# Performance work log

Measured on AMD Instinct MI355X. Metric: run time of the kernel, lower is better.

The kernel has to match this reference:

```python
import jax, jax.numpy as jnp
import numpy as np

# Sizes
N, T, P, D = 1000, 4, 10, 13          # nodes, point types, edge types (T*(T+1)/2), basis dim per point
F, H, EA, K, E = 128, 128, 16, 64, 20000  # node feat, edge hidden, edge attr/feat, edge op bottleneck, edges
I_NODE = D * (D + 1) // 2             # 91: symmetric ('ij=ji') self-block irreps dim
I_EDGE = D * D                        # 169: generic ('ij') block irreps dim
AVG_NEIGH = 20.0


def setup_inputs() -> dict:
    ks = jax.random.split(jax.random.key(0), 16)
    Fin = H + 2 * F                   # edge-op input: [edge_msg, node_h_i, node_h_j]
    return {
        'node_feats': jax.random.normal(ks[0], (N, F), jnp.float32),
        'node_attrs': jax.random.uniform(ks[1], (N, T), dtype=jnp.float32),
        'edge_feats': jax.random.normal(ks[2], (E, EA), jnp.float32),
        'edge_attrs': jax.random.normal(ks[3], (E, EA), jnp.float32),
        'edge_index': jax.random.randint(ks[4], (2, E), 0, N),
        'node_types': jax.random.randint(ks[5], (N,), 0, T),
        'edge_types': jax.random.randint(ks[6], (E,), 0, P),
        'W_msg': jax.random.normal(ks[7], (F, F), jnp.float32) / np.float32(np.sqrt(F)),
        'W_attr': jax.random.normal(ks[8], (T, F), jnp.float32) / np.float32(np.sqrt(T)),
        'W_em': jax.random.normal(ks[9], (2 * F + 2 * EA, H), jnp.float32) / np.float32(np.sqrt(2 * F + 2 * EA)),
        'W_proj': jax.random.normal(ks[10], (Fin, K), jnp.float32) / np.float32(np.sqrt(Fin)),
        'W_node': jax.random.normal(ks[11], (T, F, I_NODE), jnp.float32) / np.float32(np.sqrt(F)),
        'W_edge': jax.random.normal(ks[12], (P, K, I_EDGE), jnp.float32) / np.float32(np.sqrt(K)),
        'cob_node': jax.random.normal(ks[13], (T, I_NODE, D, D), jnp.float32) / np.float32(D),
        'cob_edge': jax.random.normal(ks[14], (P, I_EDGE, D, D), jnp.float32) / np.float32(D),
    }


def reference(node_feats, node_attrs, edge_feats, edge_attrs, edge_index, node_types,
              edge_types, W_msg, W_attr, W_em, W_proj, W_node, W_edge, cob_node, cob_edge):
    src, dst = edge_index[0], edge_index[1]
    # --- node message passing (NodeMessageBlock, simplified linear-aggregate form) ---
    m = node_feats @ W_msg                                             # [N, F]
    agg = jax.ops.segment_sum(m[src], dst, num_segments=N) \
        + jax.ops.segment_sum(m[dst], src, num_segments=N)             # symmetric edge list: both dirs
    node_h = node_feats + agg / AVG_NEIGH + node_attrs @ W_attr        # [N, F]
    # --- edge messages (EdgeMessageBlock, simplified) ---
    e_in = jnp.concatenate([node_h[src], node_h[dst], edge_feats, edge_attrs], axis=-1)
    edge_msg = jnp.tanh(e_in @ W_em)                                   # [E, H]
    # --- self-interaction blocks: per-type gather -> op -> einsum('ni,ixy->nxy', ., cob) ---
    node_irred = jnp.einsum('nf,nfi->ni', node_h, W_node[node_types])  # [N, I_NODE]
    node_blocks = jnp.einsum('ni,nixy->nxy', node_irred, cob_node[node_types])  # [N, D, D]
    # --- interaction blocks: per-edge-type op + change of basis, transpose-symmetrized ---
    onehot = jax.nn.one_hot(edge_types, P, dtype=node_feats.dtype)     # [E, P] type selector

    def edge_block(a, b):
        h = jnp.concatenate([edge_msg, a, b], axis=-1) @ W_proj        # [E, K]
        irr = jnp.einsum('epi,ep->ei', jnp.einsum('ek,pki->epi', h, W_edge), onehot)  # [E, I_EDGE]
        return jnp.einsum('epxy,ep->exy', jnp.einsum('ei,pixy->epxy', irr, cob_edge), onehot)  # [E, D, D]

    blk_ij = edge_block(node_h[src], node_h[dst])
    blk_ji = edge_block(node_h[dst], node_h[src])
    edge_blocks = 0.5 * (blk_ij + jnp.swapaxes(blk_ji, -1, -2))        # symm_transpose
    # --- scatter blocks into the dense symmetric block matrix ---
    off = jnp.arange(D)
    nidx = jnp.arange(N)[:, None] * D + off                            # [N, D] diagonal block rows/cols
    rs = src[:, None] * D + off                                        # [E, D]
    cs = dst[:, None] * D + off
    M = jnp.zeros((N * D, N * D), node_feats.dtype)
    M = M.at[nidx[:, :, None], nidx[:, None, :]].add(node_blocks)
    M = M.at[rs[:, :, None], cs[:, None, :]].add(edge_blocks)
    M = M.at[cs[:, :, None], rs[:, None, :]].add(jnp.swapaxes(edge_blocks, -1, -2))
    return M
```

## Files before the change

kernel.cpp:

```cpp
#include <hip/hip_runtime.h>
#include <cmath>

#define NN   1000
#define TT   4
#define PP   10
#define DD   13
#define FF   128
#define HH   128
#define EAA  16
#define KDIM 64
#define EE   20000
#define I_NODE 91
#define I_EDGE 169
#define MROW  13000
#define OUT_FLOAT4 42250000L

#define WS_M     0L
#define WS_AGG   128000L
#define WS_V1    256000L
#define WS_V2    384000L
#define WS_U     512000L
#define WS_HMSG  640000L
#define WS_WCOMB 1920000L
#define WS_WNC   2028160L

#define NB_CE   640
#define NB_CN   512
#define NB_MSG  1000
#define NB_FRONT (NB_CE + NB_CN + NB_MSG)

__global__ __launch_bounds__(256) void k_front(
    const float* __restrict__ We, const float* __restrict__ cobE,
    const float* __restrict__ Wn, const float* __restrict__ cobN,
    const float* __restrict__ nf, const float* __restrict__ Wmsg,
    float* __restrict__ Wcomb, float* __restrict__ Wnc,
    float* __restrict__ m, float* __restrict__ agg) {
  int b = blockIdx.x, t = threadIdx.x;
  if (b < NB_CE) {
    if (t < I_EDGE) {
      int pk = b, p = pk >> 6;
      float acc = 0.f;
      const float* wrow = We + pk * I_EDGE;
      const float* crow = cobE + p * I_EDGE * I_EDGE + t;
      for (int i = 0; i < I_EDGE; ++i) acc += wrow[i] * crow[i * I_EDGE];
      Wcomb[pk * I_EDGE + t] = acc;
    }
  } else if (b < NB_CE + NB_CN) {
    if (t < I_EDGE) {
      int tf = b - NB_CE, ty = tf >> 7;
      float acc = 0.f;
      const float* wrow = Wn + tf * I_NODE;
      const float* crow = cobN + ty * I_NODE * I_EDGE + t;
      for (int i = 0; i < I_NODE; ++i) acc += wrow[i] * crow[i * I_EDGE];
      Wnc[tf * I_EDGE + t] = acc;
    }
  } else {
    int n = b - (NB_CE + NB_CN);
    __shared__ float row[FF];
    if (t < FF) row[t] = nf[n * FF + t];
    __syncthreads();
    if (t < FF) {
      float acc = 0.f;
#pragma unroll 8
      for (int f = 0; f < FF; ++f) acc += row[f] * Wmsg[f * FF + t];
      m[n * FF + t] = acc;
    } else {
      agg[n * FF + (t - FF)] = 0.f;
    }
  }
}

#define NB_Z 8192
#define NB_SC ((EE * FF) / 256)

__global__ __launch_bounds__(256) void k_zero_scatter(
    float4* __restrict__ Mz, const float* __restrict__ m,
    const int* __restrict__ src, const int* __restrict__ dst,
    float* __restrict__ agg) {
  int b = blockIdx.x, t = threadIdx.x;
  if (b < NB_Z) {
    long base = (long)b * 256 + t;
    const long stride = (long)NB_Z * 256;
    const float4 z = make_float4(0.f, 0.f, 0.f, 0.f);
    for (long i = base; i < OUT_FLOAT4; i += stride) Mz[i] = z;
  } else {
    int idx = (b - NB_Z) * 256 + t;
    int e = idx >> 7, j = idx & 127;
    int s = src[e], d = dst[e];
    atomicAdd(&agg[d * FF + j], m[s * FF + j]);
    atomicAdd(&agg[s * FF + j], m[d * FF + j]);
  }
}

__global__ __launch_bounds__(192) void k_nodes(
    const float* __restrict__ nf, const float* __restrict__ agg,
    const float* __restrict__ na, const float* __restrict__ Wattr,
    const float* __restrict__ Wem, const float* __restrict__ Wproj,
    const int* __restrict__ ntype, const float* __restrict__ Wnc,
    float* __restrict__ V1, float* __restrict__ V2, float* __restrict__ U,
    float* __restrict__ M) {
  int n = blockIdx.x, t = threadIdx.x;
  int ty = ntype[n];
  __shared__ float row[FF];
  if (t < FF) {
    float a = 0.f;
#pragma unroll
    for (int q = 0; q < TT; ++q) a += na[n * TT + q] * Wattr[q * FF + t];
    row[t] = nf[n * FF + t] + agg[n * FF + t] * (1.0f / 20.0f) + a;
  }
  __syncthreads();
  if (t < FF) {
    float v1 = 0.f, v2 = 0.f;
#pragma unroll 4
    for (int f = 0; f < FF; ++f) {
      float x = row[f];
      v1 += x * Wem[f * HH + t];
      v2 += x * Wem[(FF + f) * HH + t];
    }
    V1[n * HH + t] = v1;
    V2[n * HH + t] = v2;
    int k = t & 63, half = t >> 6;
    const float* W = Wproj + (FF + half * FF) * KDIM + k;
    float u = 0.f;
#pragma unroll 4
    for (int f = 0; f < FF; ++f) u += row[f] * W[f * KDIM];
    U[n * 128 + t] = u;
  }
  if (t < I_EDGE) {
    float acc = 0.f;
    const float* W = Wnc + ty * FF * I_EDGE + t;
#pragma unroll 4
    for (int f = 0; f < FF; ++f) acc += row[f] * W[f * I_EDGE];
    int x = t / DD, y = t % DD;
    atomicAdd(&M[(size_t)(n * DD + x) * MROW + (n * DD + y)], acc);
  }
}

#define EPB 8
__global__ __launch_bounds__(128) void k_edge_msg(
    const float* __restrict__ V1, const float* __restrict__ V2,
    const float* __restrict__ ef, const float* __restrict__ ea,
    const int* __restrict__ src, const int* __restrict__ dst,
    const float* __restrict__ Wem, const float* __restrict__ Wproj,
    float* __restrict__ hmsg) {
  int e0 = blockIdx.x * EPB;
  int j = threadIdx.x;
  __shared__ float efa[EPB][32];
  __shared__ float em[EPB][HH];
  for (int i = j; i < EPB * 32; i += 128) {
    int e = i >> 5, c = i & 31;
    efa[e][c] = (c < 16) ? ef[(e0 + e) * EAA + c] : ea[(e0 + e) * EAA + (c - 16)];
  }
  __syncthreads();
  float wcol[32];
#pragma unroll
  for (int c = 0; c < 32; ++c) wcol[c] = Wem[(256 + c) * HH + j];
#pragma unroll
  for (int e = 0; e < EPB; ++e) {
    int s = src[e0 + e], d = dst[e0 + e];
    float acc = V1[s * HH + j] + V2[d * HH + j];
#pragma unroll
    for (int c = 0; c < 32; ++c) acc += efa[e][c] * wcol[c];
    em[e][j] = tanhf(acc);
  }
  __syncthreads();
  int k = j & 63, half = j >> 6;
  float a0 = 0.f, a1 = 0.f, a2 = 0.f, a3 = 0.f;
  for (int f = 0; f < HH; f += 4) {
    float4 m0 = *(const float4*)&em[half + 0][f];
    float4 m1 = *(const float4*)&em[half + 2][f];
    float4 m2 = *(const float4*)&em[half + 4][f];
    float4 m3 = *(const float4*)&em[half + 6][f];
    float w0 = Wproj[(f + 0) * KDIM + k], w1 = Wproj[(f + 1) * KDIM + k];
    float w2 = Wproj[(f + 2) * KDIM + k], w3 = Wproj[(f + 3) * KDIM + k];
    a0 += m0.x * w0 + m0.y * w1 + m0.z * w2 + m0.w * w3;
    a1 += m1.x * w0 + m1.y * w1 + m1.z * w2 + m1.w * w3;
    a2 += m2.x * w0 + m2.y * w1 + m2.z * w2 + m2.w * w3;
    a3 += m3.x * w0 + m3.y * w1 + m3.z * w2 + m3.w * w3;
  }
  hmsg[(e0 + half + 0) * KDIM + k] = a0;
  hmsg[(e0 + half + 2) * KDIM + k] = a1;
  hmsg[(e0 + half + 4) * KDIM + k] = a2;
  hmsg[(e0 + half + 6) * KDIM + k] = a3;
}

#define EB2 4
__global__ __launch_bounds__(768) void k_edge_blk(
    const float* __restrict__ U, const float* __restrict__ hmsg,
    const int* __restrict__ src, const int* __restrict__ dst,
    const int* __restrict__ etype, const float* __restrict__ Wcomb,
    float* __restrict__ M) {
  int t = threadIdx.x;
  int ei = threadIdx.y;
  int e = blockIdx.x * EB2 + ei;
  int s = src[e], d = dst[e], p = etype[e];
  __shared__ __align__(16) float h[EB2][2][KDIM];
  __shared__ __align__(16) float tji[EB2][I_EDGE];
  if (t < 128) {
    int k = t & 63, w = t >> 6;
    int a = w ? d : s, b = w ? s : d;
    h[ei][w][k] = hmsg[e * KDIM + k] + U[a * 128 + k] + U[b * 128 + 64 + k];
  }
  __syncthreads();
  float bij = 0.f, bji = 0.f;
  if (t < I_EDGE) {
    const float* W = Wcomb + p * KDIM * I_EDGE + t;
    for (int k = 0; k < KDIM; k += 4) {
      float4 hi = *(const float4*)&h[ei][0][k];
      float4 hj = *(const float4*)&h[ei][1][k];
      float w0 = W[(k + 0) * I_EDGE], w1 = W[(k + 1) * I_EDGE];
      float w2 = W[(k + 2) * I_EDGE], w3 = W[(k + 3) * I_EDGE];
      bij += hi.x * w0 + hi.y * w1 + hi.z * w2 + hi.w * w3;
      bji += hj.x * w0 + hj.y * w1 + hj.z * w2 + hj.w * w3;
    }
    tji[ei][t] = bji;
  }
  __syncthreads();
  if (t < I_EDGE) {
    int x = t / DD, y = t % DD;
    float eb = 0.5f * (bij + tji[ei][y * DD + x]);
    atomicAdd(&M[(size_t)(s * DD + x) * MROW + (d * DD + y)], eb);
    atomicAdd(&M[(size_t)(d * DD + y) * MROW + (s * DD + x)], eb);
  }
}

extern "C" void kernel_launch(void* const* d_in, const int* in_sizes, int n_in,
                              void* d_out, int out_size, void* d_ws, size_t ws_size,
                              hipStream_t stream) {
  const float* node_feats = (const float*)d_in[0];
  const float* node_attrs = (const float*)d_in[1];
  const float* edge_feats = (const float*)d_in[2];
  const float* edge_attrs = (const float*)d_in[3];
  const int*   edge_index = (const int*)d_in[4];
  const int*   node_types = (const int*)d_in[5];
  const int*   edge_types = (const int*)d_in[6];
  const float* W_msg  = (const float*)d_in[7];
  const float* W_attr = (const float*)d_in[8];
  const float* W_em   = (const float*)d_in[9];
  const float* W_proj = (const float*)d_in[10];
  const float* W_node = (const float*)d_in[11];
  const float* W_edge = (const float*)d_in[12];
  const float* cob_node = (const float*)d_in[13];
  const float* cob_edge = (const float*)d_in[14];

  float* M  = (float*)d_out;
  float* ws = (float*)d_ws;
  float* m_buf = ws + WS_M;
  float* agg   = ws + WS_AGG;
  float* V1    = ws + WS_V1;
  float* V2    = ws + WS_V2;
  float* U     = ws + WS_U;
  float* hmsg  = ws + WS_HMSG;
  float* Wcomb = ws + WS_WCOMB;
  float* Wnc   = ws + WS_WNC;

  const int* src = edge_index;
  const int* dst = edge_index + EE;

  k_front       <<<NB_FRONT, 256, 0, stream>>>(W_edge, cob_edge, W_node, cob_node,
                                               node_feats, W_msg, Wcomb, Wnc,
                                               m_buf, agg);
  k_zero_scatter<<<NB_Z + NB_SC, 256, 0, stream>>>((float4*)M, m_buf, src, dst, agg);
  k_nodes       <<<NN, 192, 0, stream>>>(node_feats, agg, node_attrs, W_attr,
                                         W_em, W_proj, node_types, Wnc,
                                         V1, V2, U, M);
  k_edge_msg    <<<EE / EPB, 128, 0, stream>>>(V1, V2, edge_feats, edge_attrs,
                                               src, dst, W_em, W_proj, hmsg);
  k_edge_blk    <<<dim3(EE / EB2), dim3(192, 4), 0, stream>>>(U, hmsg, src, dst,
                                                              edge_types, Wcomb, M);
}
```

Before: 917.4 us.

## Spread output zeroing across compute kernels and defer node-block atomics to tail

The 676 MB zero-fill of the dense output used to run in one kernel alongside the scatter. It is now split into three ranges, each handled by dedicated blocks interleaved into the scatter, node, and edge-message kernels, so the bandwidth-bound memset overlaps with compute. The node self-block atomic adds move into the final edge-block kernel, which runs after all zeroing is finished, and node features are staged in a new workspace buffer for that purpose. The trade-offs are added block-index bookkeeping and fatter blocks in the edge-message kernel (256 threads with half idle), and the overlap may be limited because the zero-fill is HBM-bound.

New measurement: 927.1 us. About the same (+1.1%).

```diff
diff --git a/kernel.cpp b/kernel.cpp
--- a/kernel.cpp
+++ b/kernel.cpp
@@ -15,14 +15,18 @@
 #define MROW  13000
 #define OUT_FLOAT4 42250000L
 
+#define P1_HI 6400000L
+#define P2_HI 12800000L
+
 #define WS_M     0L
 #define WS_AGG   128000L
-#define WS_V1    256000L
-#define WS_V2    384000L
-#define WS_U     512000L
-#define WS_HMSG  640000L
-#define WS_WCOMB 1920000L
-#define WS_WNC   2028160L
+#define WS_NH    256000L
+#define WS_V1    384000L
+#define WS_V2    512000L
+#define WS_U     640000L
+#define WS_HMSG  768000L
+#define WS_WCOMB 2048000L
+#define WS_WNC   2156160L
 
 #define NB_CE   640
 #define NB_CN   512
@@ -70,157 +74,194 @@
   }
 }
 
-#define NB_Z 8192
-#define NB_SC ((EE * FF) / 256)
-
-__global__ __launch_bounds__(256) void k_zero_scatter(
-    float4* __restrict__ Mz, const float* __restrict__ m,
-    const int* __restrict__ src, const int* __restrict__ dst,
-    float* __restrict__ agg) {
+#define NB_D2 11250
+__global__ __launch_bounds__(256) void k_scatter_z(
+    const float* __restrict__ m, const int* __restrict__ src,
+    const int* __restrict__ dst, float* __restrict__ agg,
+    float4* __restrict__ Mz) {
   int b = blockIdx.x, t = threadIdx.x;
-  if (b < NB_Z) {
-    long base = (long)b * 256 + t;
-    const long stride = (long)NB_Z * 256;
-    const float4 z = make_float4(0.f, 0.f, 0.f, 0.f);
-    for (long i = base; i < OUT_FLOAT4; i += stride) Mz[i] = z;
-  } else {
-    int idx = (b - NB_Z) * 256 + t;
+  int q = b / 9, g = b - q * 9;
+  if (g < 8) {
+    int idx = (q * 8 + g) * 256 + t;
     int e = idx >> 7, j = idx & 127;
     int s = src[e], d = dst[e];
     atomicAdd(&agg[d * FF + j], m[s * FF + j]);
     atomicAdd(&agg[s * FF + j], m[d * FF + j]);
-  }
-}
-
-__global__ __launch_bounds__(192) void k_nodes(
+  } else {
+    const float4 z = make_float4(0.f, 0.f, 0.f, 0.f);
+    for (long i = (long)q * 256 + t; i < P1_HI; i += 320000L) Mz[i] = z;
+  }
+}
+
+#define NB_D3 2250
+__global__ __launch_bounds__(256) void k_nodes_z(
     const float* __restrict__ nf, const float* __restrict__ agg,
     const float* __restrict__ na, const float* __restrict__ Wattr,
     const float* __restrict__ Wem, const float* __restrict__ Wproj,
-    const int* __restrict__ ntype, const float* __restrict__ Wnc,
-    float* __restrict__ V1, float* __restrict__ V2, float* __restrict__ U,
-    float* __restrict__ M) {
-  int n = blockIdx.x, t = threadIdx.x;
-  int ty = ntype[n];
+    float* __restrict__ nh, float* __restrict__ V1, float* __restrict__ V2,
+    float* __restrict__ U, float4* __restrict__ Mz) {
+  int b = blockIdx.x, t = threadIdx.x;
+  int q = b / 9, g = b - q * 9;
   __shared__ float row[FF];
-  if (t < FF) {
-    float a = 0.f;
+  if (g < 4) {
+    int n = q * 4 + g;
+    if (t < FF) {
+      float a = 0.f;
 #pragma unroll
-    for (int q = 0; q < TT; ++q) a += na[n * TT + q] * Wattr[q * FF + t];
-    row[t] = nf[n * FF + t] + agg[n * FF + t] * (1.0f / 20.0f) + a;
-  }
-  __syncthreads();
-  if (t < FF) {
-    float v1 = 0.f, v2 = 0.f;
+      for (int p = 0; p < TT; ++p) a += na[n * TT + p] * Wattr[p * FF + t];
+      float v = nf[n * FF + t] + agg[n * FF + t] * (1.0f / 20.0f) + a;
+      row[t] = v;
+      nh[n * FF + t] = v;
+    }
+    __syncthreads();
+    if (t < FF) {
+      float v1 = 0.f, v2 = 0.f;
 #pragma unroll 4
-    for (int f = 0; f < FF; ++f) {
-      float x = row[f];
-      v1 += x * Wem[f * HH + t];
-      v2 += x * Wem[(FF + f) * HH + t];
-    }
-    V1[n * HH + t] = v1;
-    V2[n * HH + t] = v2;
-    int k = t & 63, half = t >> 6;
-    const float* W = Wproj + (FF + half * FF) * KDIM + k;
-    float u = 0.f;
+      for (int f = 0; f < FF; ++f) {
+        float x = row[f];
+        v1 += x * Wem[f * HH + t];
+        v2 += x * Wem[(FF + f) * HH + t];
+      }
+      V1[n * HH + t] = v1;
+      V2[n * HH + t] = v2;
+      int k = t & 63, half = t >> 6;
+      const float* W = Wproj + (FF + half * FF) * KDIM + k;
+      float u = 0.f;
 #pragma unroll 4
-    for (int f = 0; f < FF; ++f) u += row[f] * W[f * KDIM];
-    U[n * 128 + t] = u;
-  }
-  if (t < I_EDGE) {
-    float acc = 0.f;
-    const float* W = Wnc + ty * FF * I_EDGE + t;
-#pragma unroll 4
-    for (int f = 0; f < FF; ++f) acc += row[f] * W[f * I_EDGE];
-    int x = t / DD, y = t % DD;
-    atomicAdd(&M[(size_t)(n * DD + x) * MROW + (n * DD + y)], acc);
+      for (int f = 0; f < FF; ++f) u += row[f] * W[f * KDIM];
+      U[n * 128 + t] = u;
+    }
+  } else {
+    int zid = q * 5 + (g - 4);
+    const float4 z = make_float4(0.f, 0.f, 0.f, 0.f);
+    for (long i = P1_HI + (long)zid * 256 + t; i < P2_HI; i += 320000L) Mz[i] = z;
   }
 }
 
 #define EPB 8
-__global__ __launch_bounds__(128) void k_edge_msg(
+#define NB_D4 8250
+__global__ __launch_bounds__(256) void k_edge_msg_z(
     const float* __restrict__ V1, const float* __restrict__ V2,
     const float* __restrict__ ef, const float* __restrict__ ea,
     const int* __restrict__ src, const int* __restrict__ dst,
     const float* __restrict__ Wem, const float* __restrict__ Wproj,
-    float* __restrict__ hmsg) {
-  int e0 = blockIdx.x * EPB;
-  int j = threadIdx.x;
+    float* __restrict__ hmsg, float4* __restrict__ Mz) {
+  int b = blockIdx.x, t = threadIdx.x;
+  int zid = -1, mi = -1;
+  if (b < 8000) {
+    int q = b >> 4, g = b & 15;
+    if (g < 5) mi = q * 5 + g;
+    else       zid = q * 11 + (g - 5);
+  } else {
+    zid = 5500 + (b - 8000);
+  }
+  if (zid >= 0) {
+    const float4 z = make_float4(0.f, 0.f, 0.f, 0.f);
+    for (long i = P2_HI + (long)zid * 256 + t; i < OUT_FLOAT4; i += 1472000L)
+      Mz[i] = z;
+    return;
+  }
+  int e0 = mi * EPB;
+  int j = t;
   __shared__ float efa[EPB][32];
   __shared__ float em[EPB][HH];
-  for (int i = j; i < EPB * 32; i += 128) {
-    int e = i >> 5, c = i & 31;
-    efa[e][c] = (c < 16) ? ef[(e0 + e) * EAA + c] : ea[(e0 + e) * EAA + (c - 16)];
+  if (j < 128) {
+    for (int i = j; i < EPB * 32; i += 128) {
+      int e = i >> 5, c = i & 31;
+      efa[e][c] = (c < 16) ? ef[(e0 + e) * EAA + c] : ea[(e0 + e) * EAA + (c - 16)];
+    }
   }
   __syncthreads();
-  float wcol[32];
+  if (j < 128) {
+    float wcol[32];
 #pragma unroll
-  for (int c = 0; c < 32; ++c) wcol[c] = Wem[(256 + c) * HH + j];
+    for (int c = 0; c < 32; ++c) wcol[c] = Wem[(256 + c) * HH + j];
 #pragma unroll
-  for (int e = 0; e < EPB; ++e) {
-    int s = src[e0 + e], d = dst[e0 + e];
-    float acc = V1[s * HH + j] + V2[d * HH + j];
+    for (int e = 0; e < EPB; ++e) {
+      int s = src[e0 + e], d = dst[e0 + e];
+      float acc = V1[s * HH + j] + V2[d * HH + j];
 #pragma unroll
-    for (int c = 0; c < 32; ++c) acc += efa[e][c] * wcol[c];
-    em[e][j] = tanhf(acc);
+      for (int c = 0; c < 32; ++c) acc += efa[e][c] * wcol[c];
+      em[e][j] = tanhf(acc);
+    }
   }
   __syncthreads();
-  int k = j & 63, half = j >> 6;
-  float a0 = 0.f, a1 = 0.f, a2 = 0.f, a3 = 0.f;
-  for (int f = 0; f < HH; f += 4) {
-    float4 m0 = *(const float4*)&em[half + 0][f];
-    float4 m1 = *(const float4*)&em[half + 2][f];
-    float4 m2 = *(const float4*)&em[half + 4][f];
-    float4 m3 = *(const float4*)&em[half + 6][f];
-    float w0 = Wproj[(f + 0) * KDIM + k], w1 = Wproj[(f + 1) * KDIM + k];
-    float w2 = Wproj[(f + 2) * KDIM + k], w3 = Wproj[(f + 3) * KDIM + k];
-    a0 += m0.x * w0 + m0.y * w1 + m0.z * w2 + m0.w * w3;
-    a1 += m1.x * w0 + m1.y * w1 + m1.z * w2 + m1.w * w3;
-    a2 += m2.x * w0 + m2.y * w1 + m2.z * w2 + m2.w * w3;
-    a3 += m3.x * w0 + m3.y * w1 + m3.z * w2 + m3.w * w3;
-  }
-  hmsg[(e0 + half + 0) * KDIM + k] = a0;
-  hmsg[(e0 + half + 2) * KDIM + k] = a1;
-  hmsg[(e0 + half + 4) * KDIM + k] = a2;
-  hmsg[(e0 + half + 6) * KDIM + k] = a3;
+  if (j < 128) {
+    int k = j & 63, half = j >> 6;
+    float a0 = 0.f, a1 = 0.f, a2 = 0.f, a3 = 0.f;
+    for (int f = 0; f < HH; f += 4) {
+      float4 m0 = *(const float4*)&em[half + 0][f];
+      float4 m1 = *(const float4*)&em[half + 2][f];
+      float4 m2 = *(const float4*)&em[half + 4][f];
+      float4 m3 = *(const float4*)&em[half + 6][f];
+      float w0 = Wproj[(f + 0) * KDIM + k], w1 = Wproj[(f + 1) * KDIM + k];
+      float w2 = Wproj[(f + 2) * KDIM + k], w3 = Wproj[(f + 3) * KDIM + k];
+      a0 += m0.x * w0 + m0.y * w1 + m0.z * w2 + m0.w * w3;
+      a1 += m1.x * w0 + m1.y * w1 + m1.z * w2 + m1.w * w3;
+      a2 += m2.x * w0 + m2.y * w1 + m2.z * w2 + m2.w * w3;
+      a3 += m3.x * w0 + m3.y * w1 + m3.z * w2 + m3.w * w3;
+    }
+    hmsg[(e0 + half + 0) * KDIM + k] = a0;
+    hmsg[(e0 + half + 2) * KDIM + k] = a1;
+    hmsg[(e0 + half + 4) * KDIM + k] = a2;
+    hmsg[(e0 + half + 6) * KDIM + k] = a3;
+  }
 }
 
 #define EB2 4
-__global__ __launch_bounds__(768) void k_edge_blk(
+__global__ __launch_bounds__(768) void k_tail(
     const float* __restrict__ U, const float* __restrict__ hmsg,
     const int* __restrict__ src, const int* __restrict__ dst,
     const int* __restrict__ etype, const float* __restrict__ Wcomb,
-    float* __restrict__ M) {
-  int t = threadIdx.x;
-  int ei = threadIdx.y;
-  int e = blockIdx.x * EB2 + ei;
-  int s = src[e], d = dst[e], p = etype[e];
+    const float* __restrict__ nh, const int* __restrict__ ntype,
+    const float* __restrict__ Wnc, float* __restrict__ M) {
+  int b = blockIdx.x, tf = threadIdx.x;
   __shared__ __align__(16) float h[EB2][2][KDIM];
   __shared__ __align__(16) float tji[EB2][I_EDGE];
-  if (t < 128) {
-    int k = t & 63, w = t >> 6;
-    int a = w ? d : s, b = w ? s : d;
-    h[ei][w][k] = hmsg[e * KDIM + k] + U[a * 128 + k] + U[b * 128 + 64 + k];
-  }
-  __syncthreads();
-  float bij = 0.f, bji = 0.f;
-  if (t < I_EDGE) {
-    const float* W = Wcomb + p * KDIM * I_EDGE + t;
-    for (int k = 0; k < KDIM; k += 4) {
-      float4 hi = *(const float4*)&h[ei][0][k];
-      float4 hj = *(const float4*)&h[ei][1][k];
-      float w0 = W[(k + 0) * I_EDGE], w1 = W[(k + 1) * I_EDGE];
-      float w2 = W[(k + 2) * I_EDGE], w3 = W[(k + 3) * I_EDGE];
-      bij += hi.x * w0 + hi.y * w1 + hi.z * w2 + hi.w * w3;
-      bji += hj.x * w0 + hj.y * w1 + hj.z * w2 + hj.w * w3;
-    }
-    tji[ei][t] = bji;
-  }
-  __syncthreads();
-  if (t < I_EDGE) {
-    int x = t / DD, y = t % DD;
-    float eb = 0.5f * (bij + tji[ei][y * DD + x]);
-    atomicAdd(&M[(size_t)(s * DD + x) * MROW + (d * DD + y)], eb);
-    atomicAdd(&M[(size_t)(d * DD + y) * MROW + (s * DD + x)], eb);
+  __shared__ float row[FF];
+  if (b < 5000) {
+    int t = tf % 192, ei = tf / 192;
+    int e = b * EB2 + ei;
+    int s = src[e], d = dst[e], p = etype[e];
+    if (t < 128) {
+      int k = t & 63, w = t >> 6;
+      int a = w ? d : s, bb = w ? s : d;
+      h[ei][w][k] = hmsg[e * KDIM + k] + U[a * 128 + k] + U[bb * 128 + 64 + k];
+    }
+    __syncthreads();
+    float bij = 0.f, bji = 0.f;
+    if (t < I_EDGE) {
+      const float* W = Wcomb + p * KDIM * I_EDGE + t;
+      for (int k = 0; k < KDIM; k += 4) {
+        float4 hi = *(const float4*)&h[ei][0][k];
+        float4 hj = *(const float4*)&h[ei][1][k];
+        float w0 = W[(k + 0) * I_EDGE], w1 = W[(k + 1) * I_EDGE];
+        float w2 = W[(k + 2) * I_EDGE], w3 = W[(k + 3) * I_EDGE];
+        bij += hi.x * w0 + hi.y * w1 + hi.z * w2 + hi.w * w3;
+        bji += hj.x * w0 + hj.y * w1 + hj.z * w2 + hj.w * w3;
+      }
+      tji[ei][t] = bji;
+    }
+    __syncthreads();
+    if (t < I_EDGE) {
+      int x = t / DD, y = t % DD;
+      float eb = 0.5f * (bij + tji[ei][y * DD + x]);
+      atomicAdd(&M[(size_t)(s * DD + x) * MROW + (d * DD + y)], eb);
+      atomicAdd(&M[(size_t)(d * DD + y) * MROW + (s * DD + x)], eb);
+    }
+  } else {
+    int n = b - 5000;
+    int ty = ntype[n];
+    if (tf < FF) row[tf] = nh[n * FF + tf];
+    __syncthreads();
+    if (tf < I_EDGE) {
+      float acc = 0.f;
+      const float* W = Wnc + ty * FF * I_EDGE + tf;
+#pragma unroll 4
+      for (int f = 0; f < FF; ++f) acc += row[f] * W[f * I_EDGE];
+      int x = tf / DD, y = tf % DD;
+      atomicAdd(&M[(size_t)(n * DD + x) * MROW + (n * DD + y)], acc);
+    }
   }
 }
 
@@ -247,6 +288,7 @@
   float* ws = (float*)d_ws;
   float* m_buf = ws + WS_M;
   float* agg   = ws + WS_AGG;
+  float* nh    = ws + WS_NH;
   float* V1    = ws + WS_V1;
   float* V2    = ws + WS_V2;
   float* U     = ws + WS_U;
@@ -257,15 +299,14 @@
   const int* src = edge_index;
   const int* dst = edge_index + EE;
 
-  k_front       <<<NB_FRONT, 256, 0, stream>>>(W_edge, cob_edge, W_node, cob_node,
-                                               node_feats, W_msg, Wcomb, Wnc,
-                                               m_buf, agg);
-  k_zero_scatter<<<NB_Z + NB_SC, 256, 0, stream>>>((float4*)M, m_buf, src, dst, agg);
-  k_nodes       <<<NN, 192, 0, stream>>>(node_feats, agg, node_attrs, W_attr,
-                                         W_em, W_proj, node_types, Wnc,
-                                         V1, V2, U, M);
-  k_edge_msg    <<<EE / EPB, 128, 0, stream>>>(V1, V2, edge_feats, edge_attrs,
-                                               src, dst, W_em, W_proj, hmsg);
-  k_edge_blk    <<<dim3(EE / EB2), dim3(192, 4), 0, stream>>>(U, hmsg, src, dst,
-                                                              edge_types, Wcomb, M);
-}
+  k_front     <<<NB_FRONT, 256, 0, stream>>>(W_edge, cob_edge, W_node, cob_node,
+                                             node_feats, W_msg, Wcomb, Wnc,
+                                             m_buf, agg);
+  k_scatter_z <<<NB_D2, 256, 0, stream>>>(m_buf, src, dst, agg, (float4*)M);
+  k_nodes_z   <<<NB_D3, 256, 0, stream>>>(node_feats, agg, node_attrs, W_attr,
+                                          W_em, W_proj, nh, V1, V2, U, (float4*)M);
+  k_edge_msg_z<<<NB_D4, 256, 0, stream>>>(V1, V2, edge_feats, edge_attrs, src, dst,
+                                          W_em, W_proj, hmsg, (float4*)M);
+  k_tail      <<<6000, 768, 0, stream>>>(U, hmsg, src, dst, edge_types, Wcomb,
+                                         nh, node_types, Wnc, M);
+}
```
